# Kernel optimization log

Measured on AMD Instinct MI355X. Metric: run time of the kernel, lower is better.

The kernel has to match this reference:

```python
import jax, jax.numpy as jnp
import numpy as np

D_IN, D, SEQ, B = 512, 1024, 2048, 8
EPS = 1e-5


def positional_encoding(seq_len, d):
    pos = np.arange(seq_len)[:, None].astype(np.float32)
    i = np.arange(d)[None, :].astype(np.float32)
    angle_rads = pos / (10000.0 ** (2.0 * np.floor(i / 2.0) / np.float32(d)))
    angle_rads[:, 0::2] = np.sin(angle_rads[:, 0::2])
    angle_rads[:, 1::2] = np.cos(angle_rads[:, 1::2])
    return jnp.asarray(angle_rads[None, ...], dtype=jnp.float32)  # [1, s, d]


def setup_inputs() -> dict:
    key = jax.random.key(0)
    ks = jax.random.split(key, 10)
    def lin(k, fan_in, shape):
        bound = 1.0 / np.sqrt(fan_in)
        return jax.random.uniform(k, shape, jnp.float32, -bound, bound)
    return {
        "inputs": jax.random.normal(ks[0], (B, SEQ, D_IN), jnp.float32),
        "embed_w": lin(ks[1], D_IN, (D, D_IN)),
        "embed_b": lin(ks[2], D_IN, (D,)),
        "wq_w": lin(ks[3], D, (D, D)), "wq_b": lin(ks[3], D, (D,)),
        "wk_w": lin(ks[4], D, (D, D)), "wk_b": lin(ks[4], D, (D,)),
        "wv_w": lin(ks[5], D, (D, D)), "wv_b": lin(ks[5], D, (D,)),
        "ln_g": jnp.ones((D,), jnp.float32),
        "ln_b": jnp.zeros((D,), jnp.float32),
        "soft_key_w": lin(ks[6], D, (D, D)),
        "soft_query": jax.random.normal(ks[7], (D,), jnp.float32),
        "pos_enc": positional_encoding(SEQ, D),
    }


def reference(inputs, embed_w, embed_b, wq_w, wq_b, wk_w, wk_b, wv_w, wv_b,
              ln_g, ln_b, soft_key_w, soft_query, pos_enc):
    x = jnp.einsum('bsi,oi->bso', inputs, embed_w) + embed_b  # embed
    x = x + pos_enc  # broadcast positional encoding over batch
    Q = jnp.einsum('bsd,od->bso', x, wq_w) + wq_b
    K = jnp.einsum('bsd,od->bso', x, wk_w) + wk_b
    V = jnp.einsum('bsd,od->bso', x, wv_w) + wv_b
    score = jnp.einsum('bso,bio->bsi', Q, K) / jnp.sqrt(jnp.float32(D))
    score = jax.nn.softmax(score, axis=2)
    Z = jnp.einsum('bsi,bio->bso', score, V)
    h = x + Z
    mu = jnp.mean(h, axis=-1, keepdims=True)
    var = jnp.mean(jnp.square(h - mu), axis=-1, keepdims=True)
    H = (h - mu) * jax.lax.rsqrt(var + EPS) * ln_g + ln_b
    soft_key = jnp.tanh(jnp.einsum('bsd,od->bso', H, soft_key_w))
    soft_score = jax.nn.softmax(jnp.einsum('bso,o->bs', soft_key, soft_query), axis=1)
    return jnp.einsum('bs,bso->bo', soft_score, H)
```

## Files before the change

kernel.cpp:

```cpp
#include <hip/hip_runtime.h>
#include <hip/hip_bf16.h>
#include <math.h>

typedef __bf16 bf16_t;
typedef bf16_t bf16x8 __attribute__((ext_vector_type(8)));
typedef bf16_t bf16x4 __attribute__((ext_vector_type(4)));
typedef float  f32x4  __attribute__((ext_vector_type(4)));

#define D_IN   512
#define DMODEL 1024
#define SEQ    2048
#define BATCH  8
#define NTOK   (BATCH*SEQ)

typedef __attribute__((address_space(1))) unsigned int gu32;
typedef __attribute__((address_space(3))) unsigned int lu32;

__device__ __forceinline__ void async16(const void* g, void* l) {
    __builtin_amdgcn_global_load_lds((gu32*)g, (lu32*)l, 16, 0, 0);
}


#define PH_DS(AB_, BB_, QM, QN)                                               \
    _Pragma("unroll")                                                         \
    for (int s_ = 0; s_ < 2; ++s_) {                                          \
        const int po_ = (((s_ << 2) | lq) ^ lr7) << 3;                        \
        _Pragma("unroll")                                                     \
        for (int t_ = 0; t_ < 4; ++t_)                                        \
            af[s_][t_] = *(const bf16x8*)&(AB_)[(wrow + (QM)*64 + t_*16 + lr)*64 + po_]; \
        _Pragma("unroll")                                                     \
        for (int u_ = 0; u_ < 2; ++u_)                                        \
            bfv[s_][u_] = *(const bf16x8*)&(BB_)[(wcol + (QN)*32 + u_*16 + lr)*64 + po_]; \
    }

#define PH_MM(QM, QN)                                                         \
    __builtin_amdgcn_s_barrier();                                             \
    asm volatile("s_waitcnt lgkmcnt(0)");                                     \
    __builtin_amdgcn_s_setprio(1);                                            \
    _Pragma("unroll")                                                         \
    for (int s_ = 0; s_ < 2; ++s_) {                                          \
        _Pragma("unroll")                                                     \
        for (int t_ = 0; t_ < 4; ++t_) {                                      \
            _Pragma("unroll")                                                 \
            for (int u_ = 0; u_ < 2; ++u_)                                    \
                acc[(QM)*4 + t_][(QN)*2 + u_] =                               \
                    __builtin_amdgcn_mfma_f32_16x16x32_bf16(af[s_][t_], bfv[s_][u_], \
                        acc[(QM)*4 + t_][(QN)*2 + u_], 0, 0, 0);              \
        }                                                                     \
    }                                                                         \
    __builtin_amdgcn_s_setprio(0);

#define PH_END                                                                \
    __builtin_amdgcn_s_barrier();                                             \
    asm volatile("" ::: "memory");

#define STAGE_A(Q, DST, KO) {                                                 \
    _Pragma("unroll")                                                         \
    for (int j_ = 0; j_ < 2; ++j_) {                                          \
        const int i_ = (wid << 1) | j_;                                       \
        const int g_ = i_ + (i_ & 8) + ((Q) << 3);                            \
        async16(Ag + (long)((g_ << 3) + srow8) * K + (KO) + sk, (DST) + (g_ << 9)); \
    } }

#define STAGE_B(Q, DST, KO) {                                                 \
    _Pragma("unroll")                                                         \
    for (int j_ = 0; j_ < 2; ++j_) {                                          \
        const int i_ = (wid << 1) | j_;                                       \
        const int g_ = (((i_ & 12) << 1) | (i_ & 3)) + ((Q) << 2);            \
        async16(Bg + (long)((g_ << 3) + srow8) * K + (KO) + sk, (DST) + (g_ << 9)); \
    } }

template<int EPI>
__global__ __launch_bounds__(512, 2)
void gemm_bt(const bf16_t* __restrict__ Ab, const bf16_t* __restrict__ Bb,
             bf16_t* __restrict__ Cb, int K, int ldc, int gx, int gy,
             long batchA, long batchB, long batchC,
             const float* __restrict__ bias, const float* __restrict__ aux_f,
             const bf16_t* __restrict__ resid, float* __restrict__ logits,
             const float* __restrict__ bias3)
{
    __shared__ __align__(16) bf16_t smem[65536];

    const int tid  = threadIdx.x;
    const int lane = tid & 63;
    const int wid  = tid >> 6;
    const int wr   = wid >> 2;
    const int wc   = wid & 3;

    const int flat = blockIdx.x;
    const int nb   = gridDim.x;
    const int vid  = (flat & 7) * (nb >> 3) + (flat >> 3);
    const int pb   = gx * gy;
    const int z    = vid / pb;
    const int w    = vid - z * pb;
    const int sy   = w / (gx * 4);
    const int r    = w - sy * (gx * 4);
    const int sx   = r >> 4;
    const int inner= r & 15;
    const int mtile = (sy * 4 + (inner & 3)) * 256;
    const int ntile = (sx * 4 + (inner >> 2)) * 256;

    const bf16_t* Ag = Ab + (long)z * batchA + (long)mtile * K;
    const bf16_t* Bg = Bb + (long)z * batchB + (long)ntile * K;

    f32x4 acc[8][4];
    #pragma unroll
    for (int i = 0; i < 8; ++i)
        #pragma unroll
        for (int j = 0; j < 4; ++j)
            acc[i][j] = (f32x4)(0.f);

    const int lr  = lane & 15;
    const int lr7 = lr & 7;
    const int lq  = lane >> 4;
    const int wrow = wr * 128;
    const int wcol = wc * 64;

    const int srow8 = lane >> 3;
    const int sk    = ((lane & 7) ^ srow8) * 8;

    bf16_t* const A0 = smem;
    bf16_t* const B0 = smem + 16384;
    bf16_t* const A1 = smem + 32768;
    bf16_t* const B1 = smem + 49152;

    const int niter = K >> 7;

    STAGE_A(0, A0, 0);  STAGE_A(1, A0, 0);
    STAGE_B(0, B0, 0);  STAGE_B(1, B0, 0);
    STAGE_A(0, A1, 64); STAGE_A(1, A1, 64);
    STAGE_B(0, B1, 64); STAGE_B(1, B1, 64);
    asm volatile("s_waitcnt vmcnt(8)" ::: "memory");
    __builtin_amdgcn_s_barrier();
    asm volatile("" ::: "memory");

    for (int it = 0; it < niter; ++it) {
        const int kb = it << 7;
        const bool nf   = (it > 0);
        const bool more = (it + 1 < niter);
        bf16x8 af[2][4], bfv[2][2];

        PH_DS(A0, B0, 0, 0);
        if (nf) { STAGE_A(1, A1, kb + 64); }
        PH_MM(0, 0); PH_END;

        PH_DS(A0, B0, 0, 1);
        if (nf) { STAGE_B(1, B1, kb + 64); }
        PH_MM(0, 1); PH_END;

        PH_DS(A0, B0, 1, 0);
        if (more) { STAGE_A(0, A0, kb + 128); }
        PH_MM(1, 0); PH_END;

        PH_DS(A0, B0, 1, 1);
        if (more) { STAGE_B(0, B0, kb + 128); }
        PH_MM(1, 1);
        if (more) asm volatile("s_waitcnt vmcnt(4)" ::: "memory");
        else      asm volatile("s_waitcnt vmcnt(0)" ::: "memory");
        PH_END;

        PH_DS(A1, B1, 0, 0);
        if (more) { STAGE_A(1, A0, kb + 128); }
        PH_MM(0, 0); PH_END;

        PH_DS(A1, B1, 0, 1);
        if (more) { STAGE_B(1, B0, kb + 128); }
        PH_MM(0, 1); PH_END;

        PH_DS(A1, B1, 1, 0);
        if (more) { STAGE_A(0, A1, kb + 192); }
        PH_MM(1, 0); PH_END;

        PH_DS(A1, B1, 1, 1);
        if (more) { STAGE_B(0, B1, kb + 192); }
        PH_MM(1, 1);
        if (more) asm volatile("s_waitcnt vmcnt(4)" ::: "memory");
        else      asm volatile("s_waitcnt vmcnt(0)" ::: "memory");
        PH_END;
    }

    if constexpr (EPI == 5) {
        const int mb = mtile + wrow + lq * 4;
        #pragma unroll
        for (int fm = 0; fm < 8; ++fm) {
            #pragma unroll
            for (int reg = 0; reg < 4; ++reg) {
                const int m = mb + fm * 16 + reg;
                float rs = 0.f;
                #pragma unroll
                for (int fn = 0; fn < 4; ++fn) {
                    const int n = ntile + wcol + fn * 16 + lr;
                    rs += tanhf(acc[fm][fn][reg]) * aux_f[n];
                }
                rs += __shfl_xor(rs, 1);
                rs += __shfl_xor(rs, 2);
                rs += __shfl_xor(rs, 4);
                rs += __shfl_xor(rs, 8);
                if (lr == 0) atomicAdd(&logits[m], rs);
            }
        }
        return;
    }

    __syncthreads();

    if constexpr (EPI == 4) {
        float* fsm = (float*)smem;
        bf16_t* C = Cb + (long)z * batchC;
        const float* rsum = bias + (long)z * SEQ;
        #pragma unroll
        for (int half = 0; half < 2; ++half) {
            if (half) __syncthreads();
            if (wr == half) {
                #pragma unroll
                for (int fm = 0; fm < 8; ++fm) {
                    #pragma unroll
                    for (int reg = 0; reg < 4; ++reg) {
                        const int rl = fm * 16 + lq * 4 + reg;
                        #pragma unroll
                        for (int fn = 0; fn < 4; ++fn) {
                            const int cl = wcol + fn * 16 + lr;
                            const int ph = (cl >> 2) ^ (rl & 31);
                            fsm[rl * 256 + (ph << 2) + (cl & 3)] = acc[fm][fn][reg];
                        }
                    }
                }
            }
            __syncthreads();
            const int chunk = tid & 31;
            const int grp   = tid >> 5;
            #pragma unroll
            for (int rep = 0; rep < 8; ++rep) {
                const int R  = grp + (rep << 4);
                const int c0 = chunk << 3;
                const int p0 = (c0 >> 2) ^ (R & 31);
                const f32x4 f0 = *(const f32x4*)&fsm[R * 256 + (p0 << 2)];
                const f32x4 f1 = *(const f32x4*)&fsm[R * 256 + ((p0 ^ 1) << 2)];
                const int Rg = half * 128 + R;
                const float inv = 1.f / rsum[mtile + Rg];
                const long off = (long)(mtile + Rg) * ldc + ntile + c0;
                const bf16x8 r8 = *(const bf16x8*)&resid[(long)z * batchC + off];
                bf16x8 val;
                #pragma unroll
                for (int i = 0; i < 4; ++i) {
                    val[i]     = (bf16_t)(f0[i] * inv + (float)r8[i]);
                    val[i + 4] = (bf16_t)(f1[i] * inv + (float)r8[i + 4]);
                }
                *(bf16x8*)&C[off] = val;
            }
        }
        return;
    }

    const int seg = (EPI == 6) ? (ntile >> 10) : 0;
    const float* bp = bias;
    if constexpr (EPI == 6) bp = (seg == 0) ? bias : (seg == 1) ? aux_f : bias3;

    #pragma unroll
    for (int fm = 0; fm < 8; ++fm) {
        #pragma unroll
        for (int reg = 0; reg < 4; ++reg) {
            const int rl = wrow + fm * 16 + lq * 4 + reg;
            #pragma unroll
            for (int fn = 0; fn < 4; ++fn) {
                const int cl = wcol + fn * 16 + lr;
                float v = acc[fm][fn][reg];
                if constexpr (EPI == 0)
                    v += bias[ntile + cl] + aux_f[((mtile + rl) & (SEQ-1))*DMODEL + ntile + cl];
                if constexpr (EPI == 3) v = __expf(v * 0.03125f);
                if constexpr (EPI == 6) v += bp[(ntile + cl) & 1023];
                smem[rl * 256 + ((((cl >> 3) ^ (rl & 7)) << 3) | (cl & 7))] = (bf16_t)v;
            }
        }
    }
    __syncthreads();

    if constexpr (EPI == 3) {
        bf16_t* C = Cb + (long)z * batchC;
        float* rsum = logits + (long)z * SEQ;
        const int chunk = tid & 31;
        const int grp   = tid >> 5;
        #pragma unroll
        for (int rep = 0; rep < 16; ++rep) {
            const int R = grp + (rep << 4);
            const int phys = chunk ^ (R & 7);
            bf16x8 val = *(const bf16x8*)&smem[R * 256 + (phys << 3)];
            const long off = (long)(mtile + R) * ldc + ntile + (chunk << 3);
            *(bf16x8*)&C[off] = val;
            float ps = 0.f;
            #pragma unroll
            for (int i = 0; i < 8; ++i) ps += (float)val[i];
            ps += __shfl_xor(ps, 1);
            ps += __shfl_xor(ps, 2);
            ps += __shfl_xor(ps, 4);
            ps += __shfl_xor(ps, 8);
            ps += __shfl_xor(ps, 16);
            if (chunk == 0) atomicAdd(&rsum[mtile + R], ps);
        }
        return;
    }

    if constexpr (EPI == 6) {
        if (seg == 2) {
            bf16_t* VTb = Cb + 33554432;
            const int col  = tid & 255;
            const int half = tid >> 8;
            const int b    = mtile >> 11, s0 = mtile & (SEQ-1);
            const long nbase = (long)b*DMODEL + (ntile & 1023) + col;
            #pragma unroll
            for (int rep = 0; rep < 16; ++rep) {
                const int R0 = half * 128 + rep * 8;
                bf16x8 o;
                #pragma unroll
                for (int i = 0; i < 8; ++i) {
                    const int rl = R0 + i;
                    o[i] = smem[rl * 256 + ((((col >> 3) ^ (rl & 7)) << 3) | (col & 7))];
                }
                *(bf16x8*)&VTb[nbase * SEQ + s0 + R0] = o;
            }
            return;
        }
        const int chunk = tid & 31;
        const int grp   = tid >> 5;
        const long base = (long)seg * 16777216 + (ntile & 1023) + (chunk << 3);
        #pragma unroll
        for (int rep = 0; rep < 16; ++rep) {
            const int R = grp + (rep << 4);
            const int phys = chunk ^ (R & 7);
            bf16x8 val = *(const bf16x8*)&smem[R * 256 + (phys << 3)];
            *(bf16x8*)&Cb[base + (long)(mtile + R) * 1024] = val;
        }
        return;
    }

    bf16_t* C = Cb + (long)z * batchC;
    const int chunk = tid & 31;
    const int grp   = tid >> 5;
    #pragma unroll
    for (int rep = 0; rep < 16; ++rep) {
        const int R = grp + (rep << 4);
        const int phys = chunk ^ (R & 7);
        bf16x8 val = *(const bf16x8*)&smem[R * 256 + (phys << 3)];
        const long off = (long)(mtile + R) * ldc + ntile + (chunk << 3);
        *(bf16x8*)&C[off] = val;
    }
}

__global__ __launch_bounds__(256) void cast_all(
        const float* __restrict__ inp, const float* __restrict__ emw,
        const float* __restrict__ wqw, const float* __restrict__ wkw,
        const float* __restrict__ wvw, const float* __restrict__ skw,
        bf16_t* __restrict__ in_b, bf16_t* __restrict__ we_b,
        bf16_t* __restrict__ wq_b, bf16_t* __restrict__ wk_b,
        bf16_t* __restrict__ wv_b, bf16_t* __restrict__ sk_b,
        float* __restrict__ logits, float* __restrict__ rowsum) {
    const int i = blockIdx.x*256 + threadIdx.x;
    const float* s; bf16_t* d; int j;
    if      (i < 2097152) { s = inp; d = in_b; j = i; }
    else if (i < 2228224) { s = emw; d = we_b; j = i - 2097152; }
    else if (i < 2490368) { s = wqw; d = wq_b; j = i - 2228224; }
    else if (i < 2752512) { s = wkw; d = wk_b; j = i - 2490368; }
    else if (i < 3014656) { s = wvw; d = wv_b; j = i - 2752512; }
    else if (i < 3276800) { s = skw; d = sk_b; j = i - 3014656; }
    else if (i < 3280896) { ((f32x4*)logits)[i - 3276800] = (f32x4)(0.f); return; }
    else                  { ((f32x4*)rowsum)[i - 3280896] = (f32x4)(0.f); return; }
    const float4 f = ((const float4*)s)[j];
    bf16x4 o;
    o[0] = (bf16_t)f.x; o[1] = (bf16_t)f.y; o[2] = (bf16_t)f.z; o[3] = (bf16_t)f.w;
    ((bf16x4*)d)[j] = o;
}

__global__ __launch_bounds__(256) void layernorm_k(const bf16_t* __restrict__ h, bf16_t* __restrict__ H,
                                                   const float* __restrict__ gam, const float* __restrict__ bet) {
    const long row = blockIdx.x;
    const bf16_t* hr = h + row*DMODEL;
    bf16_t* Hr = H + row*DMODEL;
    const int t = threadIdx.x, lane = t & 63, wave = t >> 6;
    __shared__ float sm[8];
    const bf16x4 hv = *(const bf16x4*)&hr[t*4];
    float v[4]; float s = 0.f, q = 0.f;
    #pragma unroll
    for (int j = 0; j < 4; ++j) { v[j] = (float)hv[j]; s += v[j]; q += v[j]*v[j]; }
    #pragma unroll
    for (int o = 32; o; o >>= 1) { s += __shfl_xor(s, o); q += __shfl_xor(q, o); }
    if (lane == 0) { sm[wave] = s; sm[4 + wave] = q; }
    __syncthreads();
    s = (sm[0] + sm[1]) + (sm[2] + sm[3]);
    q = (sm[4] + sm[5]) + (sm[6] + sm[7]);
    const float mu  = s * (1.f/DMODEL);
    const float var = q * (1.f/DMODEL) - mu*mu;
    const float r   = rsqrtf(var + 1e-5f);
    const float4 g4 = ((const float4*)gam)[t];
    const float4 b4 = ((const float4*)bet)[t];
    bf16x4 o4;
    o4[0] = (bf16_t)((v[0] - mu)*r*g4.x + b4.x);
    o4[1] = (bf16_t)((v[1] - mu)*r*g4.y + b4.y);
    o4[2] = (bf16_t)((v[2] - mu)*r*g4.z + b4.z);
    o4[3] = (bf16_t)((v[3] - mu)*r*g4.w + b4.w);
    *(bf16x4*)&Hr[t*4] = o4;
}

__global__ __launch_bounds__(256) void pool_partial(const float* __restrict__ logits,
                                                    const bf16_t* __restrict__ H,
                                                    float* __restrict__ part) {
    const int b = blockIdx.y;
    const int c = blockIdx.x;
    const int t = threadIdx.x, lane = t & 63, wave = t >> 6;
    __shared__ float sm[8];
    __shared__ float wsm[32];
    const float* lb = logits + b*SEQ;
    const float4 a4 = ((const float4*)lb)[t];
    const float4 c4 = ((const float4*)lb)[t + 256];
    float v[8] = {a4.x, a4.y, a4.z, a4.w, c4.x, c4.y, c4.z, c4.w};
    float mx = -3.0e38f;
    #pragma unroll
    for (int j = 0; j < 8; ++j) mx = fmaxf(mx, v[j]);
    #pragma unroll
    for (int o = 32; o; o >>= 1) mx = fmaxf(mx, __shfl_xor(mx, o));
    if (lane == 0) sm[wave] = mx;
    __syncthreads();
    mx = fmaxf(fmaxf(sm[0], sm[1]), fmaxf(sm[2], sm[3]));
    float s = 0.f;
    #pragma unroll
    for (int j = 0; j < 8; ++j) s += __expf(v[j] - mx);
    #pragma unroll
    for (int o = 32; o; o >>= 1) s += __shfl_xor(s, o);
    if (lane == 0) sm[4 + wave] = s;
    __syncthreads();
    s = (sm[4] + sm[5]) + (sm[6] + sm[7]);
    const float inv = 1.f / s;
    if (t < 32) wsm[t] = __expf(lb[c*32 + t] - mx) * inv;
    __syncthreads();

    const bf16_t* Hb = H + ((long)b*SEQ + (long)c*32)*DMODEL;
    f32x4 acc = (f32x4)(0.f);
    #pragma unroll 4
    for (int i = 0; i < 32; ++i) {
        const float wi = wsm[i];
        const bf16x4 hv = *(const bf16x4*)&Hb[(long)i*DMODEL + t*4];
        acc[0] += wi * (float)hv[0];
        acc[1] += wi * (float)hv[1];
        acc[2] += wi * (float)hv[2];
        acc[3] += wi * (float)hv[3];
    }
    *(f32x4*)&part[((long)b*64 + c)*DMODEL + t*4] = acc;
}

__global__ __launch_bounds__(256) void pool_reduce(const float* __restrict__ part,
                                                   float* __restrict__ out) {
    const int i = blockIdx.x*256 + threadIdx.x;
    const int b = i >> 10, o = i & 1023;
    const float* p = part + (long)b*64*DMODEL + o;
    float s = 0.f;
    #pragma unroll
    for (int c = 0; c < 64; ++c) s += p[c*DMODEL];
    out[i] = s;
}

extern "C" void kernel_launch(void* const* d_in, const int* in_sizes, int n_in,
                              void* d_out, int out_size, void* d_ws, size_t ws_size,
                              hipStream_t stream) {
    (void)in_sizes; (void)n_in; (void)out_size; (void)ws_size;
    const float* inp = (const float*)d_in[0];
    const float* emw = (const float*)d_in[1];
    const float* emb = (const float*)d_in[2];
    const float* wqw = (const float*)d_in[3];
    const float* wqb = (const float*)d_in[4];
    const float* wkw = (const float*)d_in[5];
    const float* wkb = (const float*)d_in[6];
    const float* wvw = (const float*)d_in[7];
    const float* wvb = (const float*)d_in[8];
    const float* lng = (const float*)d_in[9];
    const float* lnb = (const float*)d_in[10];
    const float* skw = (const float*)d_in[11];
    const float* sq  = (const float*)d_in[12];
    const float* pos = (const float*)d_in[13];
    float* out = (float*)d_out;

    char* ws = (char*)d_ws;
    bf16_t* in_b   = (bf16_t*)(ws + 0);
    bf16_t* we_b   = (bf16_t*)(ws + 16777216);
    bf16_t* wq_b   = (bf16_t*)(ws + 17825792);
    bf16_t* wk_b   = (bf16_t*)(ws + 19922944);
    bf16_t* wv_b   = (bf16_t*)(ws + 22020096);
    bf16_t* sk_b   = (bf16_t*)(ws + 24117248);
    float*  logits = (float*)(ws + 26214400);
    float*  rowsum = (float*)(ws + 26279936);
    bf16_t* xb     = (bf16_t*)(ws + 26345472);
    bf16_t* Qb     = (bf16_t*)(ws + 59899904);
    bf16_t* Kb     = (bf16_t*)(ws + 93454336);
    bf16_t* VT     = (bf16_t*)(ws + 127008768);
    bf16_t* Hb     = (bf16_t*)(ws + 160563200);
    bf16_t* Pb     = (bf16_t*)(ws + 194117632);
    float*  part   = (float*)(ws + 0);

    cast_all<<<12832, 256, 0, stream>>>(inp, emw, wqw, wkw, wvw, skw,
                                        in_b, we_b, wq_b, wk_b, wv_b, sk_b,
                                        logits, rowsum);

    gemm_bt<0><<<256, 512, 0, stream>>>(in_b, we_b, xb, D_IN, DMODEL, 4, 64,
        0, 0, 0, emb, pos, nullptr, nullptr, nullptr);
    gemm_bt<6><<<768, 512, 0, stream>>>(xb, wq_b, Qb, DMODEL, DMODEL, 12, 64,
        0, 0, 0, wqb, wkb, nullptr, nullptr, wvb);
    gemm_bt<3><<<512, 512, 0, stream>>>(Qb, Kb, Pb, DMODEL, SEQ, 8, 8,
        (long)SEQ*DMODEL, (long)SEQ*DMODEL, (long)SEQ*SEQ, nullptr, nullptr, nullptr, rowsum, nullptr);
    gemm_bt<4><<<256, 512, 0, stream>>>(Pb, VT, Qb, SEQ, DMODEL, 4, 8,
        (long)SEQ*SEQ, (long)DMODEL*SEQ, (long)SEQ*DMODEL, rowsum, nullptr, xb, nullptr, nullptr);
    layernorm_k<<<NTOK, 256, 0, stream>>>(Qb, Hb, lng, lnb);
    gemm_bt<5><<<256, 512, 0, stream>>>(Hb, sk_b, nullptr, DMODEL, 0, 4, 64,
        0, 0, 0, nullptr, sq, nullptr, logits, nullptr);
    pool_partial<<<dim3(64, BATCH), 256, 0, stream>>>(logits, Hb, part);
    pool_reduce<<<32, 256, 0, stream>>>(part, out);
}
```

Baseline: 502.4 us.

## Restructure GEMM main loop to split phases by k-substep and reuse B fragments

The 8-phase loop over LDS buffers is reorganized so each phase handles one k sub-step (s) and one M half, loading all four B fragments once per k sub-step and reusing them across both M halves. Global-to-LDS async staging is reordered and regrouped, with different vmcnt wait thresholds. The aim is to cut redundant LDS reads of B and rebalance memory issue against MFMA work. The in-flight counts and buffer-reuse timing now change, which risks correctness races if the waits are miscounted.

```diff
diff --git a/kernel.cpp b/kernel.cpp
--- a/kernel.cpp
+++ b/kernel.cpp
@@ -21,32 +21,30 @@
 }
 
 
-#define PH_DS(AB_, BB_, QM, QN)                                               \
+#define LD_B(BUF, S) {                                                        \
+    const int po_ = ((((S) << 2) | lq) ^ lr7) << 3;                           \
     _Pragma("unroll")                                                         \
-    for (int s_ = 0; s_ < 2; ++s_) {                                          \
-        const int po_ = (((s_ << 2) | lq) ^ lr7) << 3;                        \
-        _Pragma("unroll")                                                     \
-        for (int t_ = 0; t_ < 4; ++t_)                                        \
-            af[s_][t_] = *(const bf16x8*)&(AB_)[(wrow + (QM)*64 + t_*16 + lr)*64 + po_]; \
-        _Pragma("unroll")                                                     \
-        for (int u_ = 0; u_ < 2; ++u_)                                        \
-            bfv[s_][u_] = *(const bf16x8*)&(BB_)[(wcol + (QN)*32 + u_*16 + lr)*64 + po_]; \
-    }
-
-#define PH_MM(QM, QN)                                                         \
+    for (int u_ = 0; u_ < 4; ++u_)                                            \
+        bfv[S][u_] = *(const bf16x8*)&(BUF)[(wcol + u_*16 + lr)*64 + po_];    \
+    }
+
+#define LD_A(BUF, S, MH) {                                                    \
+    const int po_ = ((((S) << 2) | lq) ^ lr7) << 3;                           \
+    _Pragma("unroll")                                                         \
+    for (int t_ = 0; t_ < 4; ++t_)                                            \
+        af[t_] = *(const bf16x8*)&(BUF)[(wrow + (MH)*64 + t_*16 + lr)*64 + po_]; \
+    }
+
+#define MM(S, MH)                                                             \
     __builtin_amdgcn_s_barrier();                                             \
     asm volatile("s_waitcnt lgkmcnt(0)");                                     \
     __builtin_amdgcn_s_setprio(1);                                            \
     _Pragma("unroll")                                                         \
-    for (int s_ = 0; s_ < 2; ++s_) {                                          \
+    for (int t_ = 0; t_ < 4; ++t_) {                                          \
         _Pragma("unroll")                                                     \
-        for (int t_ = 0; t_ < 4; ++t_) {                                      \
-            _Pragma("unroll")                                                 \
-            for (int u_ = 0; u_ < 2; ++u_)                                    \
-                acc[(QM)*4 + t_][(QN)*2 + u_] =                               \
-                    __builtin_amdgcn_mfma_f32_16x16x32_bf16(af[s_][t_], bfv[s_][u_], \
-                        acc[(QM)*4 + t_][(QN)*2 + u_], 0, 0, 0);              \
-        }                                                                     \
+        for (int u_ = 0; u_ < 4; ++u_)                                        \
+            acc[(MH)*4 + t_][u_] = __builtin_amdgcn_mfma_f32_16x16x32_bf16(   \
+                af[t_], bfv[S][u_], acc[(MH)*4 + t_][u_], 0, 0, 0);           \
     }                                                                         \
     __builtin_amdgcn_s_setprio(0);
 
@@ -126,56 +124,61 @@
 
     const int niter = K >> 7;
 
-    STAGE_A(0, A0, 0);  STAGE_A(1, A0, 0);
-    STAGE_B(0, B0, 0);  STAGE_B(1, B0, 0);
-    STAGE_A(0, A1, 64); STAGE_A(1, A1, 64);
-    STAGE_B(0, B1, 64); STAGE_B(1, B1, 64);
+    STAGE_A(0, A0, 0);  STAGE_B(0, B0, 0);
+    STAGE_B(1, B0, 0);  STAGE_A(1, A0, 0);
+    STAGE_A(0, A1, 64); STAGE_B(0, B1, 64);
+    STAGE_B(1, B1, 64);
     asm volatile("s_waitcnt vmcnt(8)" ::: "memory");
     __builtin_amdgcn_s_barrier();
     asm volatile("" ::: "memory");
 
     for (int it = 0; it < niter; ++it) {
         const int kb = it << 7;
-        const bool nf   = (it > 0);
         const bool more = (it + 1 < niter);
-        bf16x8 af[2][4], bfv[2][2];
-
-        PH_DS(A0, B0, 0, 0);
-        if (nf) { STAGE_A(1, A1, kb + 64); }
-        PH_MM(0, 0); PH_END;
-
-        PH_DS(A0, B0, 0, 1);
-        if (nf) { STAGE_B(1, B1, kb + 64); }
-        PH_MM(0, 1); PH_END;
-
-        PH_DS(A0, B0, 1, 0);
-        if (more) { STAGE_A(0, A0, kb + 128); }
-        PH_MM(1, 0); PH_END;
-
-        PH_DS(A0, B0, 1, 1);
-        if (more) { STAGE_B(0, B0, kb + 128); }
-        PH_MM(1, 1);
-        if (more) asm volatile("s_waitcnt vmcnt(4)" ::: "memory");
+        bf16x8 af[4], bfv[2][4];
+
+        LD_B(B0, 0); LD_A(A0, 0, 0);
+        STAGE_A(1, A1, kb + 64);
+        MM(0, 0);
+        PH_END;
+
+        LD_B(B0, 1); LD_A(A0, 1, 0);
+        MM(1, 0);
+        asm volatile("s_waitcnt vmcnt(8)" ::: "memory");
+        PH_END;
+
+        LD_A(A0, 0, 1);
+        if (more) { STAGE_A(0, A0, kb + 128); STAGE_B(0, B0, kb + 128); }
+        MM(0, 1);
+        PH_END;
+
+        LD_A(A0, 1, 1);
+        if (more) { STAGE_B(1, B0, kb + 128); }
+        MM(1, 1);
+        if (more) asm volatile("s_waitcnt vmcnt(8)" ::: "memory");
+        else      asm volatile("s_waitcnt vmcnt(2)" ::: "memory");
+        PH_END;
+
+        LD_B(B1, 0); LD_A(A1, 0, 0);
+        if (more) { STAGE_A(1, A0, kb + 128); }
+        MM(0, 0);
+        PH_END;
+
+        LD_B(B1, 1); LD_A(A1, 1, 0);
+        MM(1, 0);
+        if (more) asm volatile("s_waitcnt vmcnt(8)" ::: "memory");
         else      asm volatile("s_waitcnt vmcnt(0)" ::: "memory");
         PH_END;
 
-        PH_DS(A1, B1, 0, 0);
-        if (more) { STAGE_A(1, A0, kb + 128); }
-        PH_MM(0, 0); PH_END;
-
-        PH_DS(A1, B1, 0, 1);
-        if (more) { STAGE_B(1, B0, kb + 128); }
-        PH_MM(0, 1); PH_END;
-
-        PH_DS(A1, B1, 1, 0);
-        if (more) { STAGE_A(0, A1, kb + 192); }
-        PH_MM(1, 0); PH_END;
-
-        PH_DS(A1, B1, 1, 1);
-        if (more) { STAGE_B(0, B1, kb + 192); }
-        PH_MM(1, 1);
-        if (more) asm volatile("s_waitcnt vmcnt(4)" ::: "memory");
-        else      asm volatile("s_waitcnt vmcnt(0)" ::: "memory");
+        LD_A(A1, 0, 1);
+        if (more) { STAGE_A(0, A1, kb + 192); STAGE_B(0, B1, kb + 192); }
+        MM(0, 1);
+        PH_END;
+
+        LD_A(A1, 1, 1);
+        if (more) { STAGE_B(1, B1, kb + 192); }
+        MM(1, 1);
+        if (more) asm volatile("s_waitcnt vmcnt(8)" ::: "memory");
         PH_END;
     }
 
```

New measurement: 479.7 us. 1.05x faster.
